# Optimization experiments

Measured on AMD Instinct MI355X. Metric: run time of the kernel, lower is better.

The kernel has to match this reference:

```python
import jax, jax.numpy as jnp
import numpy as np

NUM_USERS = 100000
NUM_ITEMS = 50000
N_NODES = NUM_USERS + NUM_ITEMS
DIM = 64
N_LAYERS = 3
NNZ = 1000000
BATCH = 4096


def setup_inputs() -> dict:
    key = jax.random.key(0)
    k = jax.random.split(key, 7)
    user_idx = jax.random.randint(k[0], (BATCH,), 0, NUM_USERS, dtype=jnp.int64 if jax.config.jax_enable_x64 else jnp.int32)
    item_idx = jax.random.randint(k[1], (BATCH,), 0, NUM_ITEMS, dtype=jnp.int64 if jax.config.jax_enable_x64 else jnp.int32)
    rows = jax.random.randint(k[2], (NNZ,), 0, N_NODES, dtype=jnp.int32)
    cols = jax.random.randint(k[3], (NNZ,), 0, N_NODES, dtype=jnp.int32)
    values = jax.random.uniform(k[4], (NNZ,), dtype=jnp.float32)
    # embeddings initialized N(0, 1/dim) as in the torch module
    user_emb = jax.random.normal(k[5], (NUM_USERS, DIM), dtype=jnp.float32) / DIM
    item_emb = jax.random.normal(k[6], (NUM_ITEMS, DIM), dtype=jnp.float32) / DIM
    return {"user_idx": user_idx, "item_idx": item_idx, "rows": rows,
            "cols": cols, "values": values, "user_emb": user_emb, "item_emb": item_emb}


def _spmm(rows, cols, values, x):
    # sparse [N,N] @ dense [N,d] via gather + segment_sum
    gathered = values[:, None] * x[cols]            # [nnz, d]
    return jax.ops.segment_sum(gathered, rows, num_segments=N_NODES)


def _propagate(rows, cols, values, user_emb, item_emb):
    all_emb = jnp.concatenate([user_emb, item_emb], axis=0)  # [N, d]
    acc = all_emb
    for _ in range(N_LAYERS):
        all_emb = _spmm(rows, cols, values, all_emb)
        acc = acc + all_emb
    light_out = acc / jnp.asarray(N_LAYERS + 1, dtype=acc.dtype)  # mean over layers
    return light_out[:NUM_USERS], light_out[NUM_USERS:]


def reference(user_idx, item_idx, rows, cols, values, user_emb, item_emb):
    all_users, all_items = _propagate(rows, cols, values, user_emb, item_emb)
    user = all_users[user_idx]                      # [B, d]
    item = all_items[item_idx]                      # [B, d]
    rating = jnp.sum(user * item, axis=1)           # [B]
    return (rating, user, item)
```

## Files before the change

### kernel.cpp

```cpp
#include <hip/hip_runtime.h>

#define NUM_USERS 100000
#define NUM_ITEMS 50000
#define N_NODES   150000
#define DIM       64
#define NNZ       1000000
#define BATCH     4096

#define BROWS  240
#define NBUCK  (N_NODES / BROWS)
#define WPB    (BROWS / 8)
#define NWG    256
#define CHUNK  ((NNZ + NWG - 1) / NWG)
#define SCAN_N (NBUCK * NWG)
#define SCAN_B 512
#define NBLK_S ((SCAN_N + SCAN_B - 1) / SCAN_B)

#define NWAVES (NBUCK * WPB)
#define NBINS  32
#define ESCAP  4096
#define PACKED_CAP 3000000

typedef unsigned int uint32;

__device__ __forceinline__ ushort f2bf(float f) {
    uint32 u = __float_as_uint(f);
    u += 0x7FFFu + ((u >> 16) & 1u);
    return (ushort)(u >> 16);
}
__device__ __forceinline__ float bf2f(ushort u) {
    return __uint_as_float(((uint32)u) << 16);
}

__global__ __launch_bounds__(256) void count_kernel(const int* __restrict__ rows,
                                                    int* __restrict__ cntArr) {
    __shared__ int h[NBUCK];
    for (int k = threadIdx.x; k < NBUCK; k += 256) h[k] = 0;
    __syncthreads();
    int lo = blockIdx.x * CHUNK, hi = min(NNZ, lo + CHUNK);
    for (int e = lo + threadIdx.x; e < hi; e += 256)
        atomicAdd(&h[__builtin_nontemporal_load(&rows[e]) / BROWS], 1);
    __syncthreads();
    for (int k = threadIdx.x; k < NBUCK; k += 256)
        cntArr[k * NWG + blockIdx.x] = h[k];
}

__global__ __launch_bounds__(SCAN_B) void scan_block_kernel(
        const int* __restrict__ in, int* __restrict__ out,
        int* __restrict__ blksum, int n) {
    __shared__ int sh[SCAN_B];
    int i = blockIdx.x * SCAN_B + threadIdx.x;
    int v = (i < n) ? in[i] : 0;
    sh[threadIdx.x] = v;
    __syncthreads();
    for (int off = 1; off < SCAN_B; off <<= 1) {
        int t = (threadIdx.x >= off) ? sh[threadIdx.x - off] : 0;
        __syncthreads();
        sh[threadIdx.x] += t;
        __syncthreads();
    }
    if (i < n) out[i] = sh[threadIdx.x] - v;
    if (threadIdx.x == SCAN_B - 1) blksum[blockIdx.x] = sh[SCAN_B - 1];
}

__global__ __launch_bounds__(SCAN_B) void scan_top_kernel(int* __restrict__ blksum,
                                                          int nblk) {
    __shared__ int sh[SCAN_B];
    int v = (threadIdx.x < nblk) ? blksum[threadIdx.x] : 0;
    sh[threadIdx.x] = v;
    __syncthreads();
    for (int off = 1; off < SCAN_B; off <<= 1) {
        int t = (threadIdx.x >= off) ? sh[threadIdx.x - off] : 0;
        __syncthreads();
        sh[threadIdx.x] += t;
        __syncthreads();
    }
    if (threadIdx.x < nblk) blksum[threadIdx.x] = sh[threadIdx.x] - v;
}

__global__ void scan_fix_kernel(int* __restrict__ out,
                                const int* __restrict__ blksum, int n,
                                int* __restrict__ rowptr,
                                int* __restrict__ gcur) {
    int i = blockIdx.x * blockDim.x + threadIdx.x;
    if (i < n) out[i] += blksum[i / SCAN_B];
    if (i == 0) { rowptr[N_NODES] = NNZ; gcur[0] = 0; }
}

__global__ __launch_bounds__(256) void scatter_lds_kernel(
        const int* __restrict__ rows,
        const int* __restrict__ cols,
        const float* __restrict__ vals,
        const int* __restrict__ baseArr,
        int2* __restrict__ ebuf) {
    __shared__ int cur[NBUCK];
    for (int k = threadIdx.x; k < NBUCK; k += 256)
        cur[k] = baseArr[k * NWG + blockIdx.x];
    __syncthreads();
    int lo = blockIdx.x * CHUNK, hi = min(NNZ, lo + CHUNK);
    for (int e = lo + threadIdx.x; e < hi; e += 256) {
        int   r = __builtin_nontemporal_load(&rows[e]);
        int   c = __builtin_nontemporal_load(&cols[e]);
        float v = __builtin_nontemporal_load(&vals[e]);
        int   b = r / BROWS;
        int pos = atomicAdd(&cur[b], 1);
        ebuf[pos] = make_int2(((r - b * BROWS) << 18) | c, __float_as_int(v));
    }
}

__global__ __launch_bounds__(256) void buildpack_kernel(
        const int* __restrict__ baseArr,
        const int2* __restrict__ ebuf,
        int2* __restrict__ ebuf2,
        int* __restrict__ rowptr,
        int* __restrict__ perm,
        int* __restrict__ tw,
        int* __restrict__ twb,
        int2* __restrict__ packed,
        int* __restrict__ gcur) {
    __shared__ int  cnt[BROWS];
    __shared__ int  rowofs[BROWS];
    __shared__ int  cur[BROWS];
    __shared__ int  sh[256];
    __shared__ int2 es[ESCAP];
    __shared__ int  sr[BROWS];
    __shared__ int  binc[NBINS];
    __shared__ int  binb[NBINS];
    __shared__ int  twq[WPB];
    __shared__ int  lofs[WPB];
    __shared__ int  baseSh;

    const int b   = blockIdx.x;
    const int tid = threadIdx.x;
    const int start = baseArr[b * NWG];
    const int end   = (b == NBUCK - 1) ? NNZ : baseArr[(b + 1) * NWG];
    const int m     = end - start;

    for (int k = tid; k < BROWS; k += 256) cnt[k] = 0;
    if (tid < NBINS) binc[tid] = 0;
    __syncthreads();

    for (int e = start + tid; e < end; e += 256)
        atomicAdd(&cnt[ebuf[e].x >> 18], 1);
    __syncthreads();

    int v = (tid < BROWS) ? cnt[tid] : 0;
    sh[tid] = v;
    __syncthreads();
    for (int off = 1; off < 256; off <<= 1) {
        int t = (tid >= off) ? sh[tid - off] : 0;
        __syncthreads();
        sh[tid] += t;
        __syncthreads();
    }
    if (tid < BROWS) {
        int p = sh[tid] - v;
        rowofs[tid] = p;
        cur[tid] = p;
        rowptr[b * BROWS + tid] = start + p;
    }
    __syncthreads();

    for (int e = start + tid; e < end; e += 256) {
        int2 p = ebuf[e];
        int row8 = p.x >> 18;
        int col  = p.x & 0x3FFFF;
        int pos = atomicAdd(&cur[row8], 1);
        if (pos < ESCAP) es[pos] = make_int2(col, p.y);
    }
    __syncthreads();
    for (int k = tid; k < m; k += 256) ebuf2[start + k] = es[k];

    if (tid < BROWS) atomicAdd(&binc[min(cnt[tid], NBINS - 1)], 1);
    __syncthreads();
    if (tid == 0) {
        int s = 0;
        for (int k = 0; k < NBINS; ++k) { binb[k] = s; s += binc[k]; binc[k] = 0; }
    }
    __syncthreads();
    if (tid < BROWS) {
        int bin = min(cnt[tid], NBINS - 1);
        int idx = atomicAdd(&binc[bin], 1);
        sr[binb[bin] + idx] = tid;
    }
    __syncthreads();

    if (tid < WPB) {
        int T = 0;
        #pragma unroll
        for (int j = 0; j < 8; ++j) T = max(T, cnt[sr[8 * tid + j]]);
        twq[tid] = T;
    }
    __syncthreads();
    if (tid == 0) {
        int s = 0;
        for (int q = 0; q < WPB; ++q) { lofs[q] = s; s += twq[q]; }
        baseSh = atomicAdd(gcur, s);
    }
    __syncthreads();
    const int base = baseSh;

    if (tid < WPB) {
        tw[b * WPB + tid]  = twq[tid];
        twb[b * WPB + tid] = base + lofs[tid];
    }
    if (tid < BROWS) perm[b * BROWS + tid] = b * BROWS + sr[tid];

    for (int q = 0; q < WPB; ++q) {
        int T = twq[q];
        int64_t bq = (int64_t)(base + lofs[q]) * 8;
        for (int idx = tid; idx < 8 * T; idx += 256) {
            int t = idx >> 3, j = idx & 7;
            int row8 = sr[8 * q + j];
            int d = cnt[row8];
            int2 ed = (t < d) ? es[rowofs[row8] + t] : make_int2(0, 0);
            packed[bq + idx] = ed;
        }
    }
}

__global__ void convert_kernel(const float* __restrict__ user_emb,
                               const float* __restrict__ item_emb,
                               ushort* __restrict__ xb) {
    const int64_t total4 = (int64_t)N_NODES * DIM / 4;
    const int64_t user4  = (int64_t)NUM_USERS * DIM / 4;
    int64_t stride = (int64_t)gridDim.x * blockDim.x;
    for (int64_t i = (int64_t)blockIdx.x * blockDim.x + threadIdx.x;
         i < total4; i += stride) {
        float4 v = (i < user4) ? ((const float4*)user_emb)[i]
                               : ((const float4*)item_emb)[i - user4];
        ushort4 o;
        o.x = f2bf(v.x); o.y = f2bf(v.y); o.z = f2bf(v.z); o.w = f2bf(v.w);
        ((ushort4*)xb)[i] = o;
    }
}

__global__ __launch_bounds__(256) void spmm8p_kernel(
        const int* __restrict__ perm,
        const int* __restrict__ twb,
        const int* __restrict__ tw,
        const int2* __restrict__ packed,
        const ushort* __restrict__ xin,
        ushort* __restrict__ yout) {
    int w = (int)((blockIdx.x * blockDim.x + threadIdx.x) >> 6);
    if (w >= NWAVES) return;
    const int lane = threadIdx.x & 63;
    const int j    = lane >> 3;
    const int sub8 = lane & 7;
    const int T = tw[w];
    const int64_t base = (int64_t)twb[w] * 8;
    const int rowv = perm[8 * w + j];
    const uint4* __restrict__ x4 = (const uint4*)xin;

    float acc[8] = {0.f, 0.f, 0.f, 0.f, 0.f, 0.f, 0.f, 0.f};

    #define DO_TRIP(tt)                                                        \
    {                                                                          \
        int   colsel = __shfl(ed.x, (tt) * 8 + j, 64);                         \
        float valsel = __uint_as_float((uint32)__shfl(ed.y, (tt) * 8 + j, 64));\
        uint4 u = x4[(uint32)colsel * 8 + sub8];                               \
        acc[0] = fmaf(valsel, __uint_as_float(u.x << 16), acc[0]);             \
        acc[1] = fmaf(valsel, __uint_as_float(u.x & 0xFFFF0000u), acc[1]);     \
        acc[2] = fmaf(valsel, __uint_as_float(u.y << 16), acc[2]);             \
        acc[3] = fmaf(valsel, __uint_as_float(u.y & 0xFFFF0000u), acc[3]);     \
        acc[4] = fmaf(valsel, __uint_as_float(u.z << 16), acc[4]);             \
        acc[5] = fmaf(valsel, __uint_as_float(u.z & 0xFFFF0000u), acc[5]);     \
        acc[6] = fmaf(valsel, __uint_as_float(u.w << 16), acc[6]);             \
        acc[7] = fmaf(valsel, __uint_as_float(u.w & 0xFFFF0000u), acc[7]);     \
    }

    int t0 = 0;
    for (; t0 + 8 <= T; t0 += 8) {
        int2 ed = packed[base + (int64_t)t0 * 8 + lane];
        DO_TRIP(0) DO_TRIP(1) DO_TRIP(2) DO_TRIP(3)
        DO_TRIP(4) DO_TRIP(5) DO_TRIP(6) DO_TRIP(7)
    }
    if (t0 < T) {
        int2 ed = packed[base + (int64_t)t0 * 8 + lane];
        int rem = T - t0;
        for (int tt = 0; tt < rem; ++tt) DO_TRIP(tt)
    }
    #undef DO_TRIP

    uint4 o;
    o.x = (uint32)f2bf(acc[0]) | ((uint32)f2bf(acc[1]) << 16);
    o.y = (uint32)f2bf(acc[2]) | ((uint32)f2bf(acc[3]) << 16);
    o.z = (uint32)f2bf(acc[4]) | ((uint32)f2bf(acc[5]) << 16);
    o.w = (uint32)f2bf(acc[6]) | ((uint32)f2bf(acc[7]) << 16);
    ((uint4*)yout)[(uint32)rowv * 8 + sub8] = o;
}

__global__ __launch_bounds__(256) void spmm_batch_kernel(
        const int* __restrict__ user_idx,
        const int* __restrict__ item_idx,
        const int* __restrict__ rowptr,
        const int2* __restrict__ edges,
        const ushort* __restrict__ xin,
        float* __restrict__ l3) {
    const int lane = threadIdx.x & 63;
    const int w = (int)(((uint32)blockIdx.x * blockDim.x + threadIdx.x) >> 6);
    const int i0 = w * 8;
    if (i0 >= 2 * BATCH) return;

    int e[8], end[8];
    int trips = 0;
    #pragma unroll
    for (int j = 0; j < 8; ++j) {
        int i = i0 + j;
        int row = (i < BATCH) ? user_idx[i] : (NUM_USERS + item_idx[i - BATCH]);
        e[j]   = rowptr[row];
        end[j] = rowptr[row + 1];
        trips = max(trips, end[j] - e[j]);
    }
    float a[8] = {0.f, 0.f, 0.f, 0.f, 0.f, 0.f, 0.f, 0.f};

    for (int t = 0; t < trips; ++t) {
        int   col[8];
        float val[8];
        #pragma unroll
        for (int j = 0; j < 8; ++j) {
            bool act = e[j] < end[j];
            int idx  = __builtin_amdgcn_readfirstlane(act ? e[j] : 0);
            int2 ed  = edges[idx];
            col[j] = __builtin_amdgcn_readfirstlane(ed.x);
            val[j] = act ? __int_as_float(ed.y) : 0.f;
            e[j]  += act ? 1 : 0;
        }
        #pragma unroll
        for (int j = 0; j < 8; ++j) {
            float xv = bf2f(xin[(int64_t)col[j] * DIM + lane]);
            a[j] = fmaf(val[j], xv, a[j]);
        }
    }
    #pragma unroll
    for (int j = 0; j < 8; ++j)
        l3[(int64_t)(i0 + j) * DIM + lane] = a[j];
}

__global__ __launch_bounds__(256) void out_fused_kernel(
        const int* __restrict__ user_idx,
        const int* __restrict__ item_idx,
        const float* __restrict__ user_emb,
        const float* __restrict__ item_emb,
        const ushort* __restrict__ l1,
        const ushort* __restrict__ l2,
        const float* __restrict__ l3,
        float* __restrict__ out) {
    const int lane = threadIdx.x & 63;
    const int b = (int)(((uint32)blockIdx.x * blockDim.x + threadIdx.x) >> 6);
    if (b >= BATCH) return;
    int u  = user_idx[b];
    int it = item_idx[b];
    int64_t ur = (int64_t)u * DIM + lane;
    int64_t ir = (int64_t)(NUM_USERS + it) * DIM + lane;
    float uv = (user_emb[ur] + bf2f(l1[ur]) + bf2f(l2[ur])
                + l3[(int64_t)b * DIM + lane]) * 0.25f;
    float iv = (item_emb[(int64_t)it * DIM + lane] + bf2f(l1[ir]) + bf2f(l2[ir])
                + l3[(int64_t)(BATCH + b) * DIM + lane]) * 0.25f;
    out[(int64_t)BATCH + (int64_t)b * DIM + lane] = uv;
    out[(int64_t)BATCH + (int64_t)BATCH * DIM + (int64_t)b * DIM + lane] = iv;
    float p = uv * iv;
    #pragma unroll
    for (int off = 32; off >= 1; off >>= 1) p += __shfl_down(p, off, 64);
    if (lane == 0) out[b] = p;
}

extern "C" void kernel_launch(void* const* d_in, const int* in_sizes, int n_in,
                              void* d_out, int out_size, void* d_ws, size_t ws_size,
                              hipStream_t stream) {
    const int*   user_idx = (const int*)  d_in[0];
    const int*   item_idx = (const int*)  d_in[1];
    const int*   rows     = (const int*)  d_in[2];
    const int*   cols     = (const int*)  d_in[3];
    const float* vals     = (const float*)d_in[4];
    const float* user_emb = (const float*)d_in[5];
    const float* item_emb = (const float*)d_in[6];
    float*       out      = (float*)d_out;

    char* base = (char*)d_ws;
    size_t off = 0;
    auto alloc = [&](size_t bytes) -> char* {
        char* p = base + off;
        off = (off + bytes + 255) & ~(size_t)255;
        return p;
    };
    int*    cntArr  = (int*)   alloc((size_t)SCAN_N * sizeof(int));
    int*    baseArr = (int*)   alloc((size_t)SCAN_N * sizeof(int));
    int*    blksum  = (int*)   alloc((size_t)(NBLK_S + 1) * sizeof(int));
    int*    rowptr  = (int*)   alloc((size_t)(N_NODES + 1) * sizeof(int));
    int*    gcur    = (int*)   alloc((size_t)64 * sizeof(int));
    int2*   ebuf    = (int2*)  alloc((size_t)NNZ * sizeof(int2));
    int2*   ebuf2   = (int2*)  alloc((size_t)NNZ * sizeof(int2));
    int2*   packed  = (int2*)  alloc((size_t)PACKED_CAP * sizeof(int2));
    int*    perm    = (int*)   alloc((size_t)N_NODES * sizeof(int));
    int*    tw      = (int*)   alloc((size_t)NWAVES * sizeof(int));
    int*    twb     = (int*)   alloc((size_t)NWAVES * sizeof(int));
    ushort* xb      = (ushort*)alloc((size_t)N_NODES * DIM * sizeof(ushort));
    ushort* buf0    = (ushort*)alloc((size_t)N_NODES * DIM * sizeof(ushort));
    ushort* buf1    = (ushort*)alloc((size_t)N_NODES * DIM * sizeof(ushort));
    float*  l3buf   = (float*) alloc((size_t)2 * BATCH * DIM * sizeof(float));

    const int TB = 256;

    count_kernel<<<NWG, TB, 0, stream>>>(rows, cntArr);
    scan_block_kernel<<<NBLK_S, SCAN_B, 0, stream>>>(cntArr, baseArr, blksum, SCAN_N);
    scan_top_kernel<<<1, SCAN_B, 0, stream>>>(blksum, NBLK_S);
    scan_fix_kernel<<<(SCAN_N + TB - 1) / TB, TB, 0, stream>>>(
        baseArr, blksum, SCAN_N, rowptr, gcur);
    scatter_lds_kernel<<<NWG, TB, 0, stream>>>(rows, cols, vals, baseArr, ebuf);
    buildpack_kernel<<<NBUCK, TB, 0, stream>>>(
        baseArr, ebuf, ebuf2, rowptr, perm, tw, twb, packed, gcur);

    convert_kernel<<<2048, TB, 0, stream>>>(user_emb, item_emb, xb);

    const int spmmBlocks = (NWAVES * 64 + TB - 1) / TB;
    spmm8p_kernel<<<spmmBlocks, TB, 0, stream>>>(perm, twb, tw, packed, xb, buf0);
    spmm8p_kernel<<<spmmBlocks, TB, 0, stream>>>(perm, twb, tw, packed, buf0, buf1);

    const int batchBlocks = (2 * BATCH / 8 * 64 + TB - 1) / TB;
    spmm_batch_kernel<<<batchBlocks, TB, 0, stream>>>(
        user_idx, item_idx, rowptr, ebuf2, buf1, l3buf);

    out_fused_kernel<<<(BATCH * 64 + TB - 1) / TB, TB, 0, stream>>>(
        user_idx, item_idx, user_emb, item_emb, buf0, buf1, l3buf, out);
}
```

Baseline: 135.3 us.

## Fuse count with convert, fold scan fixup into consumers, merge batch and output kernels

Runs the embedding-to-bf16 conversion in the same grid as the bucket-count kernel, so both share one launch and can overlap. Removes the scan-fix kernel by having scatter and buildpack add the block-sum offset when they read it. Merges the last-layer batch SpMM with the output combine, which drops the l3 intermediate buffer and one launch. It also loads the packed edges in the SpMM as nontemporal 64-bit values. Together these cut about three kernel launches and some global traffic, at the cost of more work per thread in the merged kernels.

New measurement: 128.9 us (median of 2 runs). 1.05x faster.

```diff
diff --git a/kernel.cpp b/kernel.cpp
--- a/kernel.cpp
+++ b/kernel.cpp
@@ -20,6 +20,7 @@
 #define NBINS  32
 #define ESCAP  4096
 #define PACKED_CAP 3000000
+#define CVB    2048
 
 typedef unsigned int uint32;
 
@@ -32,17 +33,35 @@
     return __uint_as_float(((uint32)u) << 16);
 }
 
-__global__ __launch_bounds__(256) void count_kernel(const int* __restrict__ rows,
-                                                    int* __restrict__ cntArr) {
+__global__ __launch_bounds__(256) void count_convert_kernel(
+        const int* __restrict__ rows,
+        int* __restrict__ cntArr,
+        const float* __restrict__ user_emb,
+        const float* __restrict__ item_emb,
+        ushort* __restrict__ xb) {
     __shared__ int h[NBUCK];
-    for (int k = threadIdx.x; k < NBUCK; k += 256) h[k] = 0;
-    __syncthreads();
-    int lo = blockIdx.x * CHUNK, hi = min(NNZ, lo + CHUNK);
-    for (int e = lo + threadIdx.x; e < hi; e += 256)
-        atomicAdd(&h[__builtin_nontemporal_load(&rows[e]) / BROWS], 1);
-    __syncthreads();
-    for (int k = threadIdx.x; k < NBUCK; k += 256)
-        cntArr[k * NWG + blockIdx.x] = h[k];
+    if (blockIdx.x < NWG) {
+        for (int k = threadIdx.x; k < NBUCK; k += 256) h[k] = 0;
+        __syncthreads();
+        int lo = blockIdx.x * CHUNK, hi = min(NNZ, lo + CHUNK);
+        for (int e = lo + threadIdx.x; e < hi; e += 256)
+            atomicAdd(&h[__builtin_nontemporal_load(&rows[e]) / BROWS], 1);
+        __syncthreads();
+        for (int k = threadIdx.x; k < NBUCK; k += 256)
+            cntArr[k * NWG + blockIdx.x] = h[k];
+    } else {
+        const int64_t total4 = (int64_t)N_NODES * DIM / 4;
+        const int64_t user4  = (int64_t)NUM_USERS * DIM / 4;
+        int64_t stride = (int64_t)CVB * 256;
+        for (int64_t i = (int64_t)(blockIdx.x - NWG) * 256 + threadIdx.x;
+             i < total4; i += stride) {
+            float4 v = (i < user4) ? ((const float4*)user_emb)[i]
+                                   : ((const float4*)item_emb)[i - user4];
+            ushort4 o;
+            o.x = f2bf(v.x); o.y = f2bf(v.y); o.z = f2bf(v.z); o.w = f2bf(v.w);
+            ((ushort4*)xb)[i] = o;
+        }
+    }
 }
 
 __global__ __launch_bounds__(SCAN_B) void scan_block_kernel(
@@ -64,7 +83,9 @@
 }
 
 __global__ __launch_bounds__(SCAN_B) void scan_top_kernel(int* __restrict__ blksum,
-                                                          int nblk) {
+                                                          int nblk,
+                                                          int* __restrict__ rowptr,
+                                                          int* __restrict__ gcur) {
     __shared__ int sh[SCAN_B];
     int v = (threadIdx.x < nblk) ? blksum[threadIdx.x] : 0;
     sh[threadIdx.x] = v;
@@ -76,15 +97,7 @@
         __syncthreads();
     }
     if (threadIdx.x < nblk) blksum[threadIdx.x] = sh[threadIdx.x] - v;
-}
-
-__global__ void scan_fix_kernel(int* __restrict__ out,
-                                const int* __restrict__ blksum, int n,
-                                int* __restrict__ rowptr,
-                                int* __restrict__ gcur) {
-    int i = blockIdx.x * blockDim.x + threadIdx.x;
-    if (i < n) out[i] += blksum[i / SCAN_B];
-    if (i == 0) { rowptr[N_NODES] = NNZ; gcur[0] = 0; }
+    if (threadIdx.x == 0) { rowptr[N_NODES] = NNZ; gcur[0] = 0; }
 }
 
 __global__ __launch_bounds__(256) void scatter_lds_kernel(
@@ -92,10 +105,13 @@
         const int* __restrict__ cols,
         const float* __restrict__ vals,
         const int* __restrict__ baseArr,
+        const int* __restrict__ blksum,
         int2* __restrict__ ebuf) {
     __shared__ int cur[NBUCK];
-    for (int k = threadIdx.x; k < NBUCK; k += 256)
-        cur[k] = baseArr[k * NWG + blockIdx.x];
+    for (int k = threadIdx.x; k < NBUCK; k += 256) {
+        int idx = k * NWG + blockIdx.x;
+        cur[k] = baseArr[idx] + blksum[idx >> 9];
+    }
     __syncthreads();
     int lo = blockIdx.x * CHUNK, hi = min(NNZ, lo + CHUNK);
     for (int e = lo + threadIdx.x; e < hi; e += 256) {
@@ -110,6 +126,7 @@
 
 __global__ __launch_bounds__(256) void buildpack_kernel(
         const int* __restrict__ baseArr,
+        const int* __restrict__ blksum,
         const int2* __restrict__ ebuf,
         int2* __restrict__ ebuf2,
         int* __restrict__ rowptr,
@@ -132,9 +149,11 @@
 
     const int b   = blockIdx.x;
     const int tid = threadIdx.x;
-    const int start = baseArr[b * NWG];
-    const int end   = (b == NBUCK - 1) ? NNZ : baseArr[(b + 1) * NWG];
-    const int m     = end - start;
+    const int i0  = b * NWG;
+    const int start = baseArr[i0] + blksum[i0 >> 9];
+    const int i1  = (b + 1) * NWG;
+    const int end = (b == NBUCK - 1) ? NNZ : (baseArr[i1] + blksum[i1 >> 9]);
+    const int m   = end - start;
 
     for (int k = tid; k < BROWS; k += 256) cnt[k] = 0;
     if (tid < NBINS) binc[tid] = 0;
@@ -219,27 +238,11 @@
     }
 }
 
-__global__ void convert_kernel(const float* __restrict__ user_emb,
-                               const float* __restrict__ item_emb,
-                               ushort* __restrict__ xb) {
-    const int64_t total4 = (int64_t)N_NODES * DIM / 4;
-    const int64_t user4  = (int64_t)NUM_USERS * DIM / 4;
-    int64_t stride = (int64_t)gridDim.x * blockDim.x;
-    for (int64_t i = (int64_t)blockIdx.x * blockDim.x + threadIdx.x;
-         i < total4; i += stride) {
-        float4 v = (i < user4) ? ((const float4*)user_emb)[i]
-                               : ((const float4*)item_emb)[i - user4];
-        ushort4 o;
-        o.x = f2bf(v.x); o.y = f2bf(v.y); o.z = f2bf(v.z); o.w = f2bf(v.w);
-        ((ushort4*)xb)[i] = o;
-    }
-}
-
 __global__ __launch_bounds__(256) void spmm8p_kernel(
         const int* __restrict__ perm,
         const int* __restrict__ twb,
         const int* __restrict__ tw,
-        const int2* __restrict__ packed,
+        const long long* __restrict__ packed,
         const ushort* __restrict__ xin,
         ushort* __restrict__ yout) {
     int w = (int)((blockIdx.x * blockDim.x + threadIdx.x) >> 6);
@@ -256,8 +259,8 @@
 
     #define DO_TRIP(tt)                                                        \
     {                                                                          \
-        int   colsel = __shfl(ed.x, (tt) * 8 + j, 64);                         \
-        float valsel = __uint_as_float((uint32)__shfl(ed.y, (tt) * 8 + j, 64));\
+        int   colsel = __shfl(edc, (tt) * 8 + j, 64);                          \
+        float valsel = __uint_as_float((uint32)__shfl(edv, (tt) * 8 + j, 64)); \
         uint4 u = x4[(uint32)colsel * 8 + sub8];                               \
         acc[0] = fmaf(valsel, __uint_as_float(u.x << 16), acc[0]);             \
         acc[1] = fmaf(valsel, __uint_as_float(u.x & 0xFFFF0000u), acc[1]);     \
@@ -271,12 +274,16 @@
 
     int t0 = 0;
     for (; t0 + 8 <= T; t0 += 8) {
-        int2 ed = packed[base + (int64_t)t0 * 8 + lane];
+        long long raw = __builtin_nontemporal_load(&packed[base + (int64_t)t0 * 8 + lane]);
+        int edc = (int)(uint32)(raw & 0xFFFFFFFFll);
+        int edv = (int)(uint32)(raw >> 32);
         DO_TRIP(0) DO_TRIP(1) DO_TRIP(2) DO_TRIP(3)
         DO_TRIP(4) DO_TRIP(5) DO_TRIP(6) DO_TRIP(7)
     }
     if (t0 < T) {
-        int2 ed = packed[base + (int64_t)t0 * 8 + lane];
+        long long raw = __builtin_nontemporal_load(&packed[base + (int64_t)t0 * 8 + lane]);
+        int edc = (int)(uint32)(raw & 0xFFFFFFFFll);
+        int edv = (int)(uint32)(raw >> 32);
         int rem = T - t0;
         for (int tt = 0; tt < rem; ++tt) DO_TRIP(tt)
     }
@@ -290,24 +297,30 @@
     ((uint4*)yout)[(uint32)rowv * 8 + sub8] = o;
 }
 
-__global__ __launch_bounds__(256) void spmm_batch_kernel(
+__global__ __launch_bounds__(256) void batch_out_kernel(
         const int* __restrict__ user_idx,
         const int* __restrict__ item_idx,
         const int* __restrict__ rowptr,
         const int2* __restrict__ edges,
         const ushort* __restrict__ xin,
-        float* __restrict__ l3) {
+        const float* __restrict__ user_emb,
+        const float* __restrict__ item_emb,
+        const ushort* __restrict__ l1,
+        const ushort* __restrict__ l2,
+        float* __restrict__ out) {
     const int lane = threadIdx.x & 63;
     const int w = (int)(((uint32)blockIdx.x * blockDim.x + threadIdx.x) >> 6);
-    const int i0 = w * 8;
-    if (i0 >= 2 * BATCH) return;
-
+    const int i0 = w * 4;
+    if (i0 >= BATCH) return;
+
+    int rowv[8];
     int e[8], end[8];
     int trips = 0;
     #pragma unroll
     for (int j = 0; j < 8; ++j) {
-        int i = i0 + j;
-        int row = (i < BATCH) ? user_idx[i] : (NUM_USERS + item_idx[i - BATCH]);
+        int row = (j < 4) ? user_idx[i0 + j]
+                          : (NUM_USERS + item_idx[i0 + j - 4]);
+        rowv[j] = row;
         e[j]   = rowptr[row];
         end[j] = rowptr[row + 1];
         trips = max(trips, end[j] - e[j]);
@@ -332,37 +345,31 @@
             a[j] = fmaf(val[j], xv, a[j]);
         }
     }
+
+    float uvv[8];
     #pragma unroll
-    for (int j = 0; j < 8; ++j)
-        l3[(int64_t)(i0 + j) * DIM + lane] = a[j];
-}
-
-__global__ __launch_bounds__(256) void out_fused_kernel(
-        const int* __restrict__ user_idx,
-        const int* __restrict__ item_idx,
-        const float* __restrict__ user_emb,
-        const float* __restrict__ item_emb,
-        const ushort* __restrict__ l1,
-        const ushort* __restrict__ l2,
-        const float* __restrict__ l3,
-        float* __restrict__ out) {
-    const int lane = threadIdx.x & 63;
-    const int b = (int)(((uint32)blockIdx.x * blockDim.x + threadIdx.x) >> 6);
-    if (b >= BATCH) return;
-    int u  = user_idx[b];
-    int it = item_idx[b];
-    int64_t ur = (int64_t)u * DIM + lane;
-    int64_t ir = (int64_t)(NUM_USERS + it) * DIM + lane;
-    float uv = (user_emb[ur] + bf2f(l1[ur]) + bf2f(l2[ur])
-                + l3[(int64_t)b * DIM + lane]) * 0.25f;
-    float iv = (item_emb[(int64_t)it * DIM + lane] + bf2f(l1[ir]) + bf2f(l2[ir])
-                + l3[(int64_t)(BATCH + b) * DIM + lane]) * 0.25f;
-    out[(int64_t)BATCH + (int64_t)b * DIM + lane] = uv;
-    out[(int64_t)BATCH + (int64_t)BATCH * DIM + (int64_t)b * DIM + lane] = iv;
-    float p = uv * iv;
+    for (int j = 0; j < 8; ++j) {
+        int row = rowv[j];
+        int64_t ro = (int64_t)row * DIM + lane;
+        float emb = (j < 4) ? user_emb[ro]
+                            : item_emb[(int64_t)(row - NUM_USERS) * DIM + lane];
+        uvv[j] = (emb + bf2f(l1[ro]) + bf2f(l2[ro]) + a[j]) * 0.25f;
+    }
     #pragma unroll
-    for (int off = 32; off >= 1; off >>= 1) p += __shfl_down(p, off, 64);
-    if (lane == 0) out[b] = p;
+    for (int j = 0; j < 4; ++j)
+        out[(int64_t)BATCH + (int64_t)(i0 + j) * DIM + lane] = uvv[j];
+    #pragma unroll
+    for (int j = 4; j < 8; ++j)
+        out[(int64_t)BATCH + (int64_t)BATCH * DIM
+            + (int64_t)(i0 + j - 4) * DIM + lane] = uvv[j];
+
+    #pragma unroll
+    for (int k = 0; k < 4; ++k) {
+        float p = uvv[k] * uvv[k + 4];
+        #pragma unroll
+        for (int off = 32; off >= 1; off >>= 1) p += __shfl_down(p, off, 64);
+        if (lane == 0) out[i0 + k] = p;
+    }
 }
 
 extern "C" void kernel_launch(void* const* d_in, const int* in_sizes, int n_in,
@@ -398,29 +405,27 @@
     ushort* xb      = (ushort*)alloc((size_t)N_NODES * DIM * sizeof(ushort));
     ushort* buf0    = (ushort*)alloc((size_t)N_NODES * DIM * sizeof(ushort));
     ushort* buf1    = (ushort*)alloc((size_t)N_NODES * DIM * sizeof(ushort));
-    float*  l3buf   = (float*) alloc((size_t)2 * BATCH * DIM * sizeof(float));
 
     const int TB = 256;
 
-    count_kernel<<<NWG, TB, 0, stream>>>(rows, cntArr);
+    count_convert_kernel<<<NWG + CVB, TB, 0, stream>>>(
+        rows, cntArr, user_emb, item_emb, xb);
+
     scan_block_kernel<<<NBLK_S, SCAN_B, 0, stream>>>(cntArr, baseArr, blksum, SCAN_N);
-    scan_top_kernel<<<1, SCAN_B, 0, stream>>>(blksum, NBLK_S);
-    scan_fix_kernel<<<(SCAN_N + TB - 1) / TB, TB, 0, stream>>>(
-        baseArr, blksum, SCAN_N, rowptr, gcur);
-    scatter_lds_kernel<<<NWG, TB, 0, stream>>>(rows, cols, vals, baseArr, ebuf);
+    scan_top_kernel<<<1, SCAN_B, 0, stream>>>(blksum, NBLK_S, rowptr, gcur);
+
+    scatter_lds_kernel<<<NWG, TB, 0, stream>>>(rows, cols, vals, baseArr, blksum, ebuf);
     buildpack_kernel<<<NBUCK, TB, 0, stream>>>(
-        baseArr, ebuf, ebuf2, rowptr, perm, tw, twb, packed, gcur);
-
-    convert_kernel<<<2048, TB, 0, stream>>>(user_emb, item_emb, xb);
+        baseArr, blksum, ebuf, ebuf2, rowptr, perm, tw, twb, packed, gcur);
 
     const int spmmBlocks = (NWAVES * 64 + TB - 1) / TB;
-    spmm8p_kernel<<<spmmBlocks, TB, 0, stream>>>(perm, twb, tw, packed, xb, buf0);
-    spmm8p_kernel<<<spmmBlocks, TB, 0, stream>>>(perm, twb, tw, packed, buf0, buf1);
-
-    const int batchBlocks = (2 * BATCH / 8 * 64 + TB - 1) / TB;
-    spmm_batch_kernel<<<batchBlocks, TB, 0, stream>>>(
-        user_idx, item_idx, rowptr, ebuf2, buf1, l3buf);
-
-    out_fused_kernel<<<(BATCH * 64 + TB - 1) / TB, TB, 0, stream>>>(
-        user_idx, item_idx, user_emb, item_emb, buf0, buf1, l3buf, out);
-}
+    spmm8p_kernel<<<spmmBlocks, TB, 0, stream>>>(
+        perm, twb, tw, (const long long*)packed, xb, buf0);
+    spmm8p_kernel<<<spmmBlocks, TB, 0, stream>>>(
+        perm, twb, tw, (const long long*)packed, buf0, buf1);
+
+    const int boBlocks = (BATCH / 4 * 64 + TB - 1) / TB;
+    batch_out_kernel<<<boBlocks, TB, 0, stream>>>(
+        user_idx, item_idx, rowptr, ebuf2, buf1,
+        user_emb, item_emb, buf0, buf1, out);
+}
```
